# Kernel tuning notes

Hardware: AMD Instinct MI355X
Metric: run time of the kernel (lower is better)

The kernel has to match this reference:

```python
import jax, jax.numpy as jnp
import numpy as np
import math

EPS = 1e-8


def _cdist(x, y):
    # torch.cdist(p=2) with a grad-safe sqrt (0 grad at zero distance)
    d2 = (jnp.sum(x * x, -1)[:, None] + jnp.sum(y * y, -1)[None, :]
          - 2.0 * x @ y.T)
    d2 = jnp.maximum(d2, 0.0)
    pos = d2 > 0
    return jnp.where(pos, jnp.sqrt(jnp.where(pos, d2, 1.0)), 0.0)


def _metric(proj, dim):
    # [B,D,D] rank-1 + identity, symmetrized, Frobenius-normalized
    m = jnp.einsum('bi,bj->bij', proj, proj) / dim
    m = m + jnp.eye(dim, dtype=proj.dtype)[None]
    m = 0.5 * (m + jnp.swapaxes(m, -2, -1))
    fro = jnp.sqrt(jnp.sum(m * m, axis=(-2, -1), keepdims=True))
    return m / (fro + EPS)


def setup_inputs() -> dict:
    key = jax.random.key(0)
    ks = jax.random.split(key, 4)
    B, D = 4096, 128
    return {
        'query_points': jax.random.normal(ks[0], (B, D), jnp.float32),
        'key_points': jax.random.normal(ks[1], (B, D), jnp.float32),
        'Wq': 0.1 * jax.random.normal(ks[2], (D, D), jnp.float32),
        'bq': jnp.zeros((D,), jnp.float32),
        'Wk': 0.1 * jax.random.normal(ks[3], (D, D), jnp.float32),
        'bk': jnp.zeros((D,), jnp.float32),
    }


def reference(query_points, key_points, Wq, bq, Wk, bk):
    D = Wq.shape[0]
    q = query_points @ Wq.T + bq  # [B,D]
    k = key_points @ Wk.T + bk    # [B,D]
    qm = _metric(q, D)            # [B,D,D]
    km = _metric(k, D)
    q_norm = jnp.sqrt(jnp.einsum('bi,bij,bj->b', q, qm, q))
    k_norm = jnp.sqrt(jnp.einsum('bi,bij,bj->b', k, km, k))
    qn = q / (q_norm[:, None] + EPS)
    kn = k / (k_norm[:, None] + EPS)
    dists = _cdist(qn, kn)                       # [B,B]
    sims = 1.0 / (1.0 + dists)
    temperature = math.sqrt(float(D))
    scores = jax.nn.softmax(sims * temperature, axis=-1)
    score_dists = _cdist(scores, scores)
    input_dists = _cdist(query_points, key_points)
    scale = jnp.mean(input_dists) / (jnp.mean(score_dists) + EPS)
    scores = scores * scale
    scores = scores / (jnp.sum(scores, axis=-1, keepdims=True) + EPS)
    return scores
```

## Files before the change

kernel.cpp:

```cpp
#include <hip/hip_runtime.h>
#include <hip/hip_bf16.h>
#include <math.h>

typedef short short8 __attribute__((ext_vector_type(8)));
typedef float floatx4 __attribute__((ext_vector_type(4)));

#define NB 4096
#define DD 128
static constexpr float EPSF = 1e-8f;
static constexpr float TEMP = 11.313708498984760390f;

static __device__ __forceinline__ short f2bf(float f) {
    __hip_bfloat16 h = __float2bfloat16(f);
    union { __hip_bfloat16 h; short s; } u; u.h = h; return u.s;
}
static __device__ __forceinline__ float bf2f(short s) {
    union { __hip_bfloat16 h; short s; } u; u.s = s;
    return __bfloat162float(u.h);
}

static __device__ __forceinline__ short8 load_cvt8(const float* __restrict__ p) {
    float4 a = *(const float4*)p;
    float4 b = *(const float4*)(p + 4);
    short8 o;
    o[0] = f2bf(a.x); o[1] = f2bf(a.y); o[2] = f2bf(a.z); o[3] = f2bf(a.w);
    o[4] = f2bf(b.x); o[5] = f2bf(b.y); o[6] = f2bf(b.z); o[7] = f2bf(b.w);
    return o;
}

__global__ __launch_bounds__(256) void proj_kernel(
    const float* __restrict__ qp, const float* __restrict__ kp,
    const float* __restrict__ Wq, const float* __restrict__ bq,
    const float* __restrict__ Wk, const float* __restrict__ bk,
    __hip_bfloat16* __restrict__ qn, __hip_bfloat16* __restrict__ kn,
    float* __restrict__ rq, float* __restrict__ rk)
{
    int t = threadIdx.x;
    int b = blockIdx.x;

    int which = b >> 7;
    int row0 = (b & 127) * 32;
    const float* x    = which ? kp : qp;
    const float* W    = which ? Wk : Wq;
    const float* bias = which ? bk : bq;
    short* outv = which ? (short*)kn : (short*)qn;
    float* outr = which ? rk : rq;

    int lane = t & 63, wid = t >> 6;
    int m = lane & 15, quad = lane >> 4;
    int colb = wid * 32;

    floatx4 acc[2][2];
    #pragma unroll
    for (int i = 0; i < 2; ++i)
        #pragma unroll
        for (int j = 0; j < 2; ++j)
            acc[i][j] = (floatx4){0.f, 0.f, 0.f, 0.f};

    #pragma unroll
    for (int ks = 0; ks < 4; ++ks) {
        int koff = ks * 32 + quad * 8;
        short8 af[2], bfr[2];
        #pragma unroll
        for (int rt = 0; rt < 2; ++rt)
            af[rt] = load_cvt8(x + (row0 + rt*16 + m) * DD + koff);
        #pragma unroll
        for (int ct = 0; ct < 2; ++ct)
            bfr[ct] = load_cvt8(W + (colb + ct*16 + m) * DD + koff);
        #pragma unroll
        for (int rt = 0; rt < 2; ++rt)
            #pragma unroll
            for (int ct = 0; ct < 2; ++ct)
                acc[rt][ct] = __builtin_amdgcn_mfma_f32_16x16x32_bf16(
                    af[rt], bfr[ct], acc[rt][ct], 0, 0, 0);
    }

    __shared__ float buf[4][32];
    __shared__ float nfb[32];

    float bv[2];
    #pragma unroll
    for (int ct = 0; ct < 2; ++ct) bv[ct] = bias[colb + ct*16 + m];

    #pragma unroll
    for (int rt = 0; rt < 2; ++rt) {
        #pragma unroll
        for (int r = 0; r < 4; ++r) {
            float p = 0.0f;
            #pragma unroll
            for (int ct = 0; ct < 2; ++ct) {
                float v = acc[rt][ct][r] + bv[ct];
                acc[rt][ct][r] = v;
                p = fmaf(v, v, p);
            }
            p += __shfl_xor(p, 1); p += __shfl_xor(p, 2);
            p += __shfl_xor(p, 4); p += __shfl_xor(p, 8);
            if (m == 0) buf[wid][rt*16 + quad*4 + r] = p;
        }
    }
    __syncthreads();
    if (t < 32) {
        float s = buf[0][t] + buf[1][t] + buf[2][t] + buf[3][t];
        float fro = sqrtf(s*s*(1.0f/16384.0f) + s*(1.0f/64.0f) + 128.0f);
        float qnorm = sqrtf((s*s*(1.0f/128.0f) + s) / (fro + EPSF));
        nfb[t] = 1.0f / (qnorm + EPSF);
    }
    __syncthreads();

    #pragma unroll
    for (int rt = 0; rt < 2; ++rt) {
        #pragma unroll
        for (int r = 0; r < 4; ++r) {
            int lrow = rt*16 + quad*4 + r;
            float nf = nfb[lrow];
            float u = 0.0f;
            #pragma unroll
            for (int ct = 0; ct < 2; ++ct) {
                float v = acc[rt][ct][r] * nf;
                short sb = f2bf(v);
                outv[(row0 + lrow) * DD + colb + ct*16 + m] = sb;
                float vf = bf2f(sb);
                u = fmaf(vf, vf, u);
            }
            u += __shfl_xor(u, 1); u += __shfl_xor(u, 2);
            u += __shfl_xor(u, 4); u += __shfl_xor(u, 8);
            if (m == 0) buf[wid][lrow] = u;
        }
    }
    __syncthreads();
    if (t < 32)
        outr[row0 + t] = buf[0][t] + buf[1][t] + buf[2][t] + buf[3][t];
}

__global__ __launch_bounds__(512) void score_rows(
    const __hip_bfloat16* __restrict__ qn, const __hip_bfloat16* __restrict__ kn,
    const float* __restrict__ rq, const float* __restrict__ rk,
    float* __restrict__ P)
{
    int lane = threadIdx.x & 63;
    int wid  = threadIdx.x >> 6;
    int m    = lane & 15;
    int quad = lane >> 4;

    int r0 = blockIdx.x * 16;
    int cs = wid * 512;

    const short* qs  = (const short*)qn;
    const short* kks = (const short*)kn;

    short8 af[4];
    #pragma unroll
    for (int k = 0; k < 4; ++k)
        af[k] = *(const short8*)(qs + (r0 + m) * DD + k*32 + quad*8);

    float rqv[4];
    #pragma unroll
    for (int r = 0; r < 4; ++r) rqv[r] = rq[r0 + quad*4 + r];

    floatx4 acc[8][4];
    float rs[4] = {0.f, 0.f, 0.f, 0.f};

    #pragma unroll
    for (int it = 0; it < 8; ++it) {
        int cb = cs + it * 64;
        #pragma unroll
        for (int ct = 0; ct < 4; ++ct) {
            int col = cb + ct*16 + m;
            short8 bfr[4];
            #pragma unroll
            for (int k = 0; k < 4; ++k)
                bfr[k] = *(const short8*)(kks + col * DD + k*32 + quad*8);
            floatx4 a = (floatx4){0.f, 0.f, 0.f, 0.f};
            #pragma unroll
            for (int k = 0; k < 4; ++k)
                a = __builtin_amdgcn_mfma_f32_16x16x32_bf16(af[k], bfr[k], a, 0, 0, 0);
            float rkv = rk[col];
            #pragma unroll
            for (int r = 0; r < 4; ++r) {
                float d2 = fmaf(-2.0f, a[r], rqv[r] + rkv);
                float d  = d2 > 0.0f ? __builtin_amdgcn_sqrtf(d2) : 0.0f;
                float e  = __expf(TEMP * __builtin_amdgcn_rcpf(1.0f + d));
                a[r] = e;
                rs[r] += e;
            }
            acc[it][ct] = a;
        }
    }

    #pragma unroll
    for (int r = 0; r < 4; ++r) {
        rs[r] += __shfl_xor(rs[r], 1); rs[r] += __shfl_xor(rs[r], 2);
        rs[r] += __shfl_xor(rs[r], 4); rs[r] += __shfl_xor(rs[r], 8);
    }

    __shared__ float sums[8][16];
    __shared__ float inv[16];
    if (m == 0) {
        #pragma unroll
        for (int r = 0; r < 4; ++r) sums[wid][quad*4 + r] = rs[r];
    }
    __syncthreads();
    if (threadIdx.x < 16) {
        float s = 0.f;
        #pragma unroll
        for (int w = 0; w < 8; ++w) s += sums[w][threadIdx.x];
        inv[threadIdx.x] = __builtin_amdgcn_rcpf(s + EPSF);
    }
    __syncthreads();

    float invv[4];
    #pragma unroll
    for (int r = 0; r < 4; ++r) invv[r] = inv[quad*4 + r];

    #pragma unroll
    for (int it = 0; it < 8; ++it) {
        int cb = cs + it * 64;
        #pragma unroll
        for (int ct = 0; ct < 4; ++ct) {
            #pragma unroll
            for (int r = 0; r < 4; ++r) {
                long row = r0 + quad*4 + r;
                P[row * NB + cb + ct*16 + m] = acc[it][ct][r] * invv[r];
            }
        }
    }
}

extern "C" void kernel_launch(void* const* d_in, const int* in_sizes, int n_in,
                              void* d_out, int out_size, void* d_ws, size_t ws_size,
                              hipStream_t stream) {
    const float* qp = (const float*)d_in[0];
    const float* kp = (const float*)d_in[1];
    const float* Wq = (const float*)d_in[2];
    const float* bq = (const float*)d_in[3];
    const float* Wk = (const float*)d_in[4];
    const float* bk = (const float*)d_in[5];
    float* P = (float*)d_out;

    char* ws = (char*)d_ws;
    __hip_bfloat16* qn = (__hip_bfloat16*)ws;
    __hip_bfloat16* kn = (__hip_bfloat16*)(ws + (size_t)NB*DD*2);
    float* rq = (float*)(ws + (size_t)NB*DD*4);
    float* rk = (float*)(ws + (size_t)NB*DD*4 + (size_t)NB*4);

    hipLaunchKernelGGL(proj_kernel, dim3(256), dim3(256), 0, stream,
                       qp, kp, Wq, bq, Wk, bk, qn, kn, rq, rk);
    hipLaunchKernelGGL(score_rows, dim3(256), dim3(512), 0, stream,
                       qn, kn, rq, rk, P);
}
```

Before: 133.2 us.

## Store q/k in MFMA fragment order and double score kernel block size

The projection kernel now writes normalized bf16 q/k rows in a pre-swizzled MFMA fragment layout, so each lane in the score kernel reads one contiguous 16-byte chunk and a wavefront reads 1 KB contiguously instead of strided rows. The score kernel moves to 1024 threads per block, with each wave covering 256 columns instead of 512. This halves the per-wave accumulator array to lower register pressure and puts more waves per row block. The cost is scattered 2-byte stores in the projection kernel and a larger cross-wave reduction.

```diff
diff --git a/kernel.cpp b/kernel.cpp
--- a/kernel.cpp
+++ b/kernel.cpp
@@ -26,6 +26,11 @@
     o[0] = f2bf(a.x); o[1] = f2bf(a.y); o[2] = f2bf(a.z); o[3] = f2bf(a.w);
     o[4] = f2bf(b.x); o[5] = f2bf(b.y); o[6] = f2bf(b.z); o[7] = f2bf(b.w);
     return o;
+}
+
+static __device__ __forceinline__ int frag_off(int g, int kidx) {
+    return ((((g >> 4) * 4 + (kidx >> 5)) * 4 + ((kidx >> 3) & 3)) * 16
+            + (g & 15)) * 8 + (kidx & 7);
 }
 
 __global__ __launch_bounds__(256) void proj_kernel(
@@ -112,13 +117,14 @@
         #pragma unroll
         for (int r = 0; r < 4; ++r) {
             int lrow = rt*16 + quad*4 + r;
+            int g = row0 + lrow;
             float nf = nfb[lrow];
             float u = 0.0f;
             #pragma unroll
             for (int ct = 0; ct < 2; ++ct) {
                 float v = acc[rt][ct][r] * nf;
                 short sb = f2bf(v);
-                outv[(row0 + lrow) * DD + colb + ct*16 + m] = sb;
+                outv[frag_off(g, colb + ct*16 + m)] = sb;
                 float vf = bf2f(sb);
                 u = fmaf(vf, vf, u);
             }
@@ -132,7 +138,7 @@
         outr[row0 + t] = buf[0][t] + buf[1][t] + buf[2][t] + buf[3][t];
 }
 
-__global__ __launch_bounds__(512) void score_rows(
+__global__ __launch_bounds__(1024) void score_rows(
     const __hip_bfloat16* __restrict__ qn, const __hip_bfloat16* __restrict__ kn,
     const float* __restrict__ rq, const float* __restrict__ rk,
     float* __restrict__ P)
@@ -142,39 +148,39 @@
     int m    = lane & 15;
     int quad = lane >> 4;
 
-    int r0 = blockIdx.x * 16;
-    int cs = wid * 512;
+    int rowblk = blockIdx.x;
+    int r0 = rowblk * 16;
+    int cs = wid * 256;
 
     const short* qs  = (const short*)qn;
     const short* kks = (const short*)kn;
 
     short8 af[4];
     #pragma unroll
-    for (int k = 0; k < 4; ++k)
-        af[k] = *(const short8*)(qs + (r0 + m) * DD + k*32 + quad*8);
+    for (int k4 = 0; k4 < 4; ++k4)
+        af[k4] = *(const short8*)(qs + ((rowblk*4 + k4)*64 + lane)*8);
 
     float rqv[4];
     #pragma unroll
     for (int r = 0; r < 4; ++r) rqv[r] = rq[r0 + quad*4 + r];
 
-    floatx4 acc[8][4];
+    floatx4 acc[4][4];
     float rs[4] = {0.f, 0.f, 0.f, 0.f};
 
     #pragma unroll
-    for (int it = 0; it < 8; ++it) {
-        int cb = cs + it * 64;
+    for (int it = 0; it < 4; ++it) {
         #pragma unroll
         for (int ct = 0; ct < 4; ++ct) {
-            int col = cb + ct*16 + m;
+            int colblk = (cs >> 4) + it*4 + ct;
             short8 bfr[4];
             #pragma unroll
-            for (int k = 0; k < 4; ++k)
-                bfr[k] = *(const short8*)(kks + col * DD + k*32 + quad*8);
+            for (int k4 = 0; k4 < 4; ++k4)
+                bfr[k4] = *(const short8*)(kks + ((colblk*4 + k4)*64 + lane)*8);
             floatx4 a = (floatx4){0.f, 0.f, 0.f, 0.f};
             #pragma unroll
-            for (int k = 0; k < 4; ++k)
-                a = __builtin_amdgcn_mfma_f32_16x16x32_bf16(af[k], bfr[k], a, 0, 0, 0);
-            float rkv = rk[col];
+            for (int k4 = 0; k4 < 4; ++k4)
+                a = __builtin_amdgcn_mfma_f32_16x16x32_bf16(af[k4], bfr[k4], a, 0, 0, 0);
+            float rkv = rk[colblk*16 + m];
             #pragma unroll
             for (int r = 0; r < 4; ++r) {
                 float d2 = fmaf(-2.0f, a[r], rqv[r] + rkv);
@@ -193,7 +199,7 @@
         rs[r] += __shfl_xor(rs[r], 4); rs[r] += __shfl_xor(rs[r], 8);
     }
 
-    __shared__ float sums[8][16];
+    __shared__ float sums[16][16];
     __shared__ float inv[16];
     if (m == 0) {
         #pragma unroll
@@ -203,7 +209,7 @@
     if (threadIdx.x < 16) {
         float s = 0.f;
         #pragma unroll
-        for (int w = 0; w < 8; ++w) s += sums[w][threadIdx.x];
+        for (int w = 0; w < 16; ++w) s += sums[w][threadIdx.x];
         inv[threadIdx.x] = __builtin_amdgcn_rcpf(s + EPSF);
     }
     __syncthreads();
@@ -213,14 +219,13 @@
     for (int r = 0; r < 4; ++r) invv[r] = inv[quad*4 + r];
 
     #pragma unroll
-    for (int it = 0; it < 8; ++it) {
-        int cb = cs + it * 64;
+    for (int it = 0; it < 4; ++it) {
         #pragma unroll
         for (int ct = 0; ct < 4; ++ct) {
             #pragma unroll
             for (int r = 0; r < 4; ++r) {
                 long row = r0 + quad*4 + r;
-                P[row * NB + cb + ct*16 + m] = acc[it][ct][r] * invv[r];
+                P[row * NB + cs + it*64 + ct*16 + m] = acc[it][ct][r] * invv[r];
             }
         }
     }
@@ -245,6 +250,6 @@
 
     hipLaunchKernelGGL(proj_kernel, dim3(256), dim3(256), 0, stream,
                        qp, kp, Wq, bq, Wk, bk, qn, kn, rq, rk);
-    hipLaunchKernelGGL(score_rows, dim3(256), dim3(512), 0, stream,
+    hipLaunchKernelGGL(score_rows, dim3(256), dim3(1024), 0, stream,
                        qn, kn, rq, rk, P);
 }
```

Result: faster. 117.0 us (-12.1%).
